# Performance work log

Measured on AMD Instinct MI355X. Metric: run time of the kernel, lower is better.

## Reference

```python
import jax, jax.numpy as jnp
import numpy as np

OUT = 7  # output_size from init


def _roi_coords(bxs, H, W, scale_h, scale_w, image_size):
    """Replicates the integer coordinate clamping logic of the torch module.
    bxs: [N,4] float (x,y,w,h). Returns int32 x1,y1,x2,y2 each [N]."""
    x, y, w, h = bxs[:, 0], bxs[:, 1], bxs[:, 2], bxs[:, 3]
    bad = (w <= 0) | (h <= 0)
    x1f = jnp.where(bad, 0.25 * image_size, x) * scale_w
    x2f = jnp.where(bad, 0.75 * image_size, x + w) * scale_w
    y1f = jnp.where(bad, 0.25 * image_size, y) * scale_h
    y2f = jnp.where(bad, 0.75 * image_size, y + h) * scale_h
    # python int() truncates toward zero -> astype(int32) does the same
    x1 = jnp.maximum(0, x1f.astype(jnp.int32))
    y1 = jnp.maximum(0, y1f.astype(jnp.int32))
    x2 = jnp.minimum(W, x2f.astype(jnp.int32) + 1)
    y2 = jnp.minimum(H, y2f.astype(jnp.int32) + 1)
    x2 = jnp.where(x2 <= x1 + 1, jnp.minimum(x1 + 2, W), x2)
    y2 = jnp.where(y2 <= y1 + 1, jnp.minimum(y1 + 2, H), y2)
    x1 = jnp.clip(x1, 0, W - 2)
    y1 = jnp.clip(y1, 0, H - 2)
    x2 = jnp.maximum(x1 + 1, jnp.minimum(x2, W))
    y2 = jnp.maximum(y1 + 1, jnp.minimum(y2, H))
    return x1, y1, x2, y2


def _bin_mask(lo, hi, L):
    """AdaptiveMaxPool2d bin membership. lo,hi: [N] int. Returns bool [N,OUT,L].
    bin k covers [lo + floor(k*sz/OUT), lo + ceil((k+1)*sz/OUT))."""
    k = jnp.arange(OUT)
    sz = hi - lo  # [N], >= 1 by construction
    s = lo[:, None] + (k[None, :] * sz[:, None]) // OUT            # [N,OUT]
    e = lo[:, None] + ((k[None, :] + 1) * sz[:, None] + OUT - 1) // OUT
    pos = jnp.arange(L)
    return (pos >= s[..., None]) & (pos < e[..., None])  # [N,OUT,L]


def _pool_image(feat, bxs, image_size):
    """feat: [C,H,W]; bxs: [N,4] -> pooled [N,C,OUT,OUT] (adaptive max per ROI)."""
    C, H, W = feat.shape
    scale_h = H / image_size
    scale_w = W / image_size
    x1, y1, x2, y2 = _roi_coords(bxs, H, W, scale_h, scale_w, image_size)
    mx = _bin_mask(x1, x2, W)  # [N,OUT,W]
    my = _bin_mask(y1, y2, H)  # [N,OUT,H]
    neg = jnp.array(-jnp.inf, feat.dtype)
    # masked max over W: [N,C,H,OUT]
    s1 = jnp.where(mx[:, None, None, :, :], feat[None, :, :, None, :], neg).max(-1)
    # masked max over H: [N,C,OUT(y),OUT(x)]
    pooled = jnp.where(my[:, None, :, :, None], s1[:, :, None, :, :], neg).max(3)
    return pooled


def setup_inputs() -> dict:
    key = jax.random.key(0)
    k1, k2, k3 = jax.random.split(key, 3)
    B, C, H, W = 1, 256, 50, 50
    N = 256  # boxes per image
    image_size = 800
    features = jax.random.normal(k1, (B, C, H, W), dtype=jnp.float32)
    xy = jax.random.uniform(k2, (B, N, 2), minval=0.0, maxval=500.0)
    wh = jax.random.uniform(k3, (B, N, 2), minval=-20.0, maxval=300.0)  # a few degenerate boxes
    boxes = jnp.concatenate([xy, wh], axis=-1).astype(jnp.float32)
    return {"features": features, "boxes": boxes, "image_size": image_size}


def reference(features, boxes, image_size):
    B, C, H, W = features.shape
    Nb = boxes.shape[1]
    pooled = jax.vmap(lambda f, bx: _pool_image(f, bx, image_size))(features, boxes)
    return pooled.reshape(B * Nb, C, OUT, OUT)
```

## Files before the change

kernel.cpp:

```cpp
#include <hip/hip_runtime.h>
#include <hip/hip_bf16.h>
#include <math.h>

#define RC   256
#define RH   50
#define RW   50
#define RN   256
#define ROUT 7

__global__ void __launch_bounds__(256)
roi_pool_kernel(const float* __restrict__ feat,
                const float* __restrict__ boxes,
                const int* __restrict__ image_size_p,
                float* __restrict__ out) {
    const int total = RN * RC * ROUT * ROUT;
    int idx = blockIdx.x * blockDim.x + threadIdx.x;
    if (idx >= total) return;

    int kx = idx % ROUT;
    int ky = (idx / ROUT) % ROUT;
    int c  = (idx / (ROUT * ROUT)) % RC;
    int n  = idx / (ROUT * ROUT * RC);

    float im = (float)(*image_size_p);
    float scale_w = (float)RW / im;
    float scale_h = (float)RH / im;

    float bx = boxes[n * 4 + 0];
    float by = boxes[n * 4 + 1];
    float bw = boxes[n * 4 + 2];
    float bh = boxes[n * 4 + 3];
    bool bad = (bw <= 0.0f) || (bh <= 0.0f);

    float x1f = (bad ? 0.25f * im : bx) * scale_w;
    float x2f = (bad ? 0.75f * im : bx + bw) * scale_w;
    float y1f = (bad ? 0.25f * im : by) * scale_h;
    float y2f = (bad ? 0.75f * im : by + bh) * scale_h;

    int x1 = max(0, (int)x1f);
    int y1 = max(0, (int)y1f);
    int x2 = min(RW, (int)x2f + 1);
    int y2 = min(RH, (int)y2f + 1);
    if (x2 <= x1 + 1) x2 = min(x1 + 2, RW);
    if (y2 <= y1 + 1) y2 = min(y1 + 2, RH);
    x1 = min(max(x1, 0), RW - 2);
    y1 = min(max(y1, 0), RH - 2);
    x2 = max(x1 + 1, min(x2, RW));
    y2 = max(y1 + 1, min(y2, RH));

    int szx = x2 - x1;
    int szy = y2 - y1;
    int sx = x1 + (kx * szx) / ROUT;
    int ex = x1 + ((kx + 1) * szx + ROUT - 1) / ROUT;
    int sy = y1 + (ky * szy) / ROUT;
    int ey = y1 + ((ky + 1) * szy + ROUT - 1) / ROUT;

    const float* __restrict__ f = feat + c * (RH * RW);
    float m = -INFINITY;
    for (int y = sy; y < ey; ++y) {
        const float* __restrict__ row = f + y * RW;
        for (int x = sx; x < ex; ++x) {
            m = fmaxf(m, row[x]);
        }
    }
    out[idx] = m;
}

extern "C" void kernel_launch(void* const* d_in, const int* in_sizes, int n_in,
                              void* d_out, int out_size, void* d_ws, size_t ws_size,
                              hipStream_t stream) {
    const float* feat  = (const float*)d_in[0];
    const float* boxes = (const float*)d_in[1];
    const int* im_sz   = (const int*)d_in[2];
    float* out = (float*)d_out;

    const int total = RN * RC * ROUT * ROUT;
    const int block = 256;
    const int grid = (total + block - 1) / block;
    roi_pool_kernel<<<grid, block, 0, stream>>>(feat, boxes, im_sz, out);
}
```

Before: 26.83 us.

## Transpose features to HWC and pool each bin across channels with float4 loads

Adds a pre-pass that transposes the feature map from CHW to HWC in workspace memory. The pool kernel then assigns one wavefront per (box, bin), with each lane covering four contiguous channels through float4 loads, so the gathers that were strided and divergent per thread become coalesced. It also stops recomputing the box coordinates per output element. The costs are an extra kernel launch, the full transpose pass, and output stores strided by 49 floats.

```diff
diff --git a/kernel.cpp b/kernel.cpp
--- a/kernel.cpp
+++ b/kernel.cpp
@@ -2,25 +2,35 @@
 #include <hip/hip_bf16.h>
 #include <math.h>
 
-#define RC   256
-#define RH   50
-#define RW   50
-#define RN   256
-#define ROUT 7
+#define RC    256
+#define RH    50
+#define RW    50
+#define RN    256
+#define ROUT  7
+#define NBINS 49
+#define HW    (RH * RW)
 
 __global__ void __launch_bounds__(256)
-roi_pool_kernel(const float* __restrict__ feat,
-                const float* __restrict__ boxes,
-                const int* __restrict__ image_size_p,
-                float* __restrict__ out) {
-    const int total = RN * RC * ROUT * ROUT;
-    int idx = blockIdx.x * blockDim.x + threadIdx.x;
-    if (idx >= total) return;
+transpose_kernel(const float* __restrict__ feat, float* __restrict__ featT) {
+    int idx = blockIdx.x * 256 + threadIdx.x;
+    int c  = idx & (RC - 1);
+    int hw = idx >> 8;
+    featT[idx] = feat[c * HW + hw];
+}
 
-    int kx = idx % ROUT;
-    int ky = (idx / ROUT) % ROUT;
-    int c  = (idx / (ROUT * ROUT)) % RC;
-    int n  = idx / (ROUT * ROUT * RC);
+__global__ void __launch_bounds__(256)
+pool_kernel(const float* __restrict__ featT,
+            const float* __restrict__ boxes,
+            const int* __restrict__ image_size_p,
+            float* __restrict__ out) {
+    int lane = threadIdx.x & 63;
+    int wv   = threadIdx.x >> 6;
+    int b    = blockIdx.x;
+    int n    = b / 13;
+    int bin  = (b % 13) * 4 + wv;
+    if (bin >= NBINS) return;
+    int ky = bin / ROUT;
+    int kx = bin % ROUT;
 
     float im = (float)(*image_size_p);
     float scale_w = (float)RW / im;
@@ -55,15 +65,24 @@
     int sy = y1 + (ky * szy) / ROUT;
     int ey = y1 + ((ky + 1) * szy + ROUT - 1) / ROUT;
 
-    const float* __restrict__ f = feat + c * (RH * RW);
-    float m = -INFINITY;
+    int c0 = lane * 4;
+    float mx_ = -INFINITY, my_ = -INFINITY, mz_ = -INFINITY, mw_ = -INFINITY;
     for (int y = sy; y < ey; ++y) {
-        const float* __restrict__ row = f + y * RW;
+        const float* __restrict__ rowp = featT + (y * RW) * RC + c0;
         for (int x = sx; x < ex; ++x) {
-            m = fmaxf(m, row[x]);
+            float4 v = *(const float4*)(rowp + x * RC);
+            mx_ = fmaxf(mx_, v.x);
+            my_ = fmaxf(my_, v.y);
+            mz_ = fmaxf(mz_, v.z);
+            mw_ = fmaxf(mw_, v.w);
         }
     }
-    out[idx] = m;
+
+    float* o = out + n * (RC * NBINS) + bin;
+    o[(c0 + 0) * NBINS] = mx_;
+    o[(c0 + 1) * NBINS] = my_;
+    o[(c0 + 2) * NBINS] = mz_;
+    o[(c0 + 3) * NBINS] = mw_;
 }
 
 extern "C" void kernel_launch(void* const* d_in, const int* in_sizes, int n_in,
@@ -72,10 +91,11 @@
     const float* feat  = (const float*)d_in[0];
     const float* boxes = (const float*)d_in[1];
     const int* im_sz   = (const int*)d_in[2];
-    float* out = (float*)d_out;
+    float* out   = (float*)d_out;
+    float* featT = (float*)d_ws;
 
-    const int total = RN * RC * ROUT * ROUT;
-    const int block = 256;
-    const int grid = (total + block - 1) / block;
-    roi_pool_kernel<<<grid, block, 0, stream>>>(feat, boxes, im_sz, out);
+    transpose_kernel<<<HW, 256, 0, stream>>>(feat, featT);
+
+    const int grid = RN * 13;
+    pool_kernel<<<grid, 256, 0, stream>>>(featT, boxes, im_sz, out);
 }
```

After: 41.45 us. 54.5% more time.

## Stage ROI rows in LDS per box and 64-channel group, reduce bins from shared memory

Applied to the files above, without the earlier changes.

Each block now handles one box and 64 channels. It streams the ROI rows in chunks of two into a padded LDS tile laid out channel-contiguous, and each wave accumulates running maxima for a strided subset of the 49 bins in registers. Results are transposed through LDS so the output writes are coalesced. This removes redundant scattered global reads of overlapping bin regions and the uncoalesced per-thread loops, at the cost of many __syncthreads rounds and a large register array per thread.

```diff
diff --git a/kernel.cpp b/kernel.cpp
--- a/kernel.cpp
+++ b/kernel.cpp
@@ -2,25 +2,32 @@
 #include <hip/hip_bf16.h>
 #include <math.h>
 
-#define RC   256
-#define RH   50
-#define RW   50
-#define RN   256
-#define ROUT 7
+#define RC    256
+#define RH    50
+#define RW    50
+#define RN    256
+#define ROUT  7
+#define NBINS 49
+#define HW    (RH * RW)
+
+#define XS    50
+#define YC    2
+#define CSTR  65
 
 __global__ void __launch_bounds__(256)
-roi_pool_kernel(const float* __restrict__ feat,
-                const float* __restrict__ boxes,
-                const int* __restrict__ image_size_p,
-                float* __restrict__ out) {
-    const int total = RN * RC * ROUT * ROUT;
-    int idx = blockIdx.x * blockDim.x + threadIdx.x;
-    if (idx >= total) return;
+roi_pool_fused(const float* __restrict__ feat,
+               const float* __restrict__ boxes,
+               const int* __restrict__ image_size_p,
+               float* __restrict__ out) {
+    __shared__ float lds[YC * XS * CSTR];
 
-    int kx = idx % ROUT;
-    int ky = (idx / ROUT) % ROUT;
-    int c  = (idx / (ROUT * ROUT)) % RC;
-    int n  = idx / (ROUT * ROUT * RC);
+    const int n    = blockIdx.x >> 2;
+    const int coff = (blockIdx.x & 3) << 6;
+    const int t    = threadIdx.x;
+    const int w    = t >> 6;
+    const int lane = t & 63;
+    const int sg   = lane >> 4;
+    const int lx   = lane & 15;
 
     float im = (float)(*image_size_p);
     float scale_w = (float)RW / im;
@@ -48,22 +55,72 @@
     x2 = max(x1 + 1, min(x2, RW));
     y2 = max(y1 + 1, min(y2, RH));
 
-    int szx = x2 - x1;
-    int szy = y2 - y1;
-    int sx = x1 + (kx * szx) / ROUT;
-    int ex = x1 + ((kx + 1) * szx + ROUT - 1) / ROUT;
-    int sy = y1 + (ky * szy) / ROUT;
-    int ey = y1 + ((ky + 1) * szy + ROUT - 1) / ROUT;
+    const int szx = x2 - x1;
+    const int szy = y2 - y1;
 
-    const float* __restrict__ f = feat + c * (RH * RW);
-    float m = -INFINITY;
-    for (int y = sy; y < ey; ++y) {
-        const float* __restrict__ row = f + y * RW;
-        for (int x = sx; x < ex; ++x) {
-            m = fmaxf(m, row[x]);
+    int sxA[13], exA[13], syA[13], eyA[13];
+    float acc[13];
+    #pragma unroll
+    for (int k = 0; k < 13; ++k) {
+        acc[k] = -INFINITY;
+        int b = w + 4 * k;
+        if (b < NBINS) {
+            int ky = b / ROUT;
+            int kx = b - ky * ROUT;
+            sxA[k] = x1 + (kx * szx) / ROUT;
+            exA[k] = x1 + ((kx + 1) * szx + ROUT - 1) / ROUT;
+            syA[k] = y1 + (ky * szy) / ROUT;
+            eyA[k] = y1 + ((ky + 1) * szy + ROUT - 1) / ROUT;
         }
     }
-    out[idx] = m;
+
+    const int nchunk = (szy + YC - 1) / YC;
+    for (int ch = 0; ch < nchunk; ++ch) {
+        const int cy0 = y1 + ch * YC;
+
+        #pragma unroll
+        for (int r = 0; r < 8; ++r) {
+            int seg = r * 16 + (w << 2) + sg;
+            int c   = seg >> 1;
+            int yy  = seg & 1;
+            int y   = cy0 + yy;
+            if (y < y2) {
+                const float* __restrict__ src = feat + (coff + c) * HW + y * RW + x1;
+                for (int x = lx; x < szx; x += 16)
+                    lds[(yy * XS + x) * CSTR + c] = src[x];
+            }
+        }
+        __syncthreads();
+
+        #pragma unroll
+        for (int k = 0; k < 13; ++k) {
+            int b = w + 4 * k;
+            if (b < NBINS) {
+                int ys = max(syA[k], cy0);
+                int ye = min(eyA[k], cy0 + YC);
+                for (int y = ys; y < ye; ++y) {
+                    int yy = y - cy0;
+                    for (int x = sxA[k]; x < exA[k]; ++x)
+                        acc[k] = fmaxf(acc[k], lds[(yy * XS + x - x1) * CSTR + lane]);
+                }
+            }
+        }
+        __syncthreads();
+    }
+
+    #pragma unroll
+    for (int k = 0; k < 13; ++k) {
+        int b = w + 4 * k;
+        if (b < NBINS) lds[b * CSTR + lane] = acc[k];
+    }
+    __syncthreads();
+
+    const int obase = (n * RC + coff) * NBINS;
+    for (int e = t; e < 64 * NBINS; e += 256) {
+        int c = e / NBINS;
+        int b = e - c * NBINS;
+        out[obase + e] = lds[b * CSTR + c];
+    }
 }
 
 extern "C" void kernel_launch(void* const* d_in, const int* in_sizes, int n_in,
@@ -74,8 +131,5 @@
     const int* im_sz   = (const int*)d_in[2];
     float* out = (float*)d_out;
 
-    const int total = RN * RC * ROUT * ROUT;
-    const int block = 256;
-    const int grid = (total + block - 1) / block;
-    roi_pool_kernel<<<grid, block, 0, stream>>>(feat, boxes, im_sz, out);
+    roi_pool_fused<<<RN * 4, 256, 0, stream>>>(feat, boxes, im_sz, out);
 }
```

Result: slower. 90.92 us (+238.9%).
